# Kernel tuning notes

Measured on AMD Instinct MI355X. Metric: run time of the kernel, lower is better.

Reference implementation:

```python
import jax, jax.numpy as jnp
import numpy as np

EPS = 1e-5
NEG_SLOPE = 0.2

def _conv1x1(x, w):
    # x: (B,C,N,K), w: (O,C) -> (B,O,N,K)
    return jnp.einsum('oc,bcnk->bonk', w, x)

def _bn(x, g, b, m, v):
    scale = g / jnp.sqrt(v + EPS)
    return x * scale[None, :, None, None] + (b - m * scale)[None, :, None, None]

def _lrelu(x):
    return jnp.where(x > 0, x, NEG_SLOPE * x)

def setup_inputs() -> dict:
    key = jax.random.key(0)
    specs = {
        'x': ((8, 6, 8192, 20), 'randn'),
        'trans_w': ((64, 6), 'randn'), 'trans_g': ((64,), 'rand'), 'trans_b': ((64,), 'randn'),
        'trans_m': ((64,), 'randn'), 'trans_v': ((64,), 'rand'),
        'pos_w1': ((64, 3), 'randn'), 'pos_g': ((64,), 'rand'), 'pos_b': ((64,), 'randn'),
        'pos_m': ((64,), 'randn'), 'pos_v': ((64,), 'rand'),
        'pos_w2': ((64, 64), 'randn'), 'pos_b2': ((64,), 'randn'),
        'gate_w1': ((16, 6), 'randn'), 'gate_g': ((16,), 'rand'), 'gate_b': ((16,), 'randn'),
        'gate_m': ((16,), 'randn'), 'gate_v': ((16,), 'rand'),
        'gate_w2': ((1, 16), 'randn'), 'gate_b2': ((1,), 'ones'),
        'attn_w1': ((16, 6), 'randn'), 'attn_g': ((16,), 'rand'), 'attn_b': ((16,), 'randn'),
        'attn_m': ((16,), 'randn'), 'attn_v': ((16,), 'rand'),
        'attn_w2': ((64, 16), 'randn'), 'attn_b2': ((64,), 'randn'),
    }
    out = {}
    for i, (name, (shape, fill)) in enumerate(specs.items()):
        k = jax.random.fold_in(key, i)
        if fill == 'randn':
            out[name] = jax.random.normal(k, shape, dtype=jnp.float32) * 0.1
        elif fill == 'rand':
            out[name] = jax.random.uniform(k, shape, dtype=jnp.float32)
        else:  # ones (gate bias init to 2.0 in original; scale ones)
            out[name] = jnp.ones(shape, dtype=jnp.float32) * 2.0
    return out

def reference(x, trans_w, trans_g, trans_b, trans_m, trans_v,
              pos_w1, pos_g, pos_b, pos_m, pos_v, pos_w2, pos_b2,
              gate_w1, gate_g, gate_b, gate_m, gate_v, gate_w2, gate_b2,
              attn_w1, attn_g, attn_b, attn_m, attn_v, attn_w2, attn_b2):
    in_channels = 3
    rel_pos = x[:, in_channels:in_channels + 3, :, :]  # (B,3,N,K)
    # pos_net: conv(3->C) + BN + LReLU + conv(C->C, bias)
    pos_h = _lrelu(_bn(_conv1x1(rel_pos, pos_w1), pos_g, pos_b, pos_m, pos_v))
    pos_enc = _conv1x1(pos_h, pos_w2) + pos_b2[None, :, None, None]
    # trans: conv(2*Cin->C) + BN + LReLU
    trans_feat = _lrelu(_bn(_conv1x1(x, trans_w), trans_g, trans_b, trans_m, trans_v)) + pos_enc
    # gate_net: conv(6->16)+BN+LReLU+conv(16->1,bias)+sigmoid (dropout=0 in eval)
    gate_h = _lrelu(_bn(_conv1x1(x, gate_w1), gate_g, gate_b, gate_m, gate_v))
    gate_map = jax.nn.sigmoid(_conv1x1(gate_h, gate_w2) + gate_b2[None, :, None, None])  # (B,1,N,K)
    clean_feat = trans_feat * gate_map
    # attn_net: conv(6->16)+BN+LReLU+conv(16->C,bias), then + pos_enc, softmax over K
    attn_h = _lrelu(_bn(_conv1x1(x, attn_w1), attn_g, attn_b, attn_m, attn_v))
    attn_logits = _conv1x1(attn_h, attn_w2) + attn_b2[None, :, None, None] + pos_enc
    attn_weights = jax.nn.softmax(attn_logits, axis=-1)
    out_attn = (trans_feat * attn_weights).sum(axis=-1)  # (B,C,N)
    out_max = clean_feat.max(axis=-1)                    # (B,C,N)
    return out_attn + out_max
```

## Files before the change

kernel.cpp:

```cpp
#include <hip/hip_runtime.h>
#include <math.h>

#define NEG 0.2f
#define EPSV 1e-5f

typedef _Float16 v8h __attribute__((ext_vector_type(8)));
typedef _Float16 v4h __attribute__((ext_vector_type(4)));
typedef float    v4f __attribute__((ext_vector_type(4)));

__device__ __forceinline__ float lrelu(float v) { return fmaxf(v, NEG * v); }

#define MFMA(a, b, c) __builtin_amdgcn_mfma_f32_16x16x32_f16((a), (b), (c), 0, 0, 0)

__global__ __launch_bounds__(256, 1)
void gsl_mfma(const float* __restrict__ x,
              const float* __restrict__ trans_w, const float* __restrict__ trans_g,
              const float* __restrict__ trans_b, const float* __restrict__ trans_m,
              const float* __restrict__ trans_v,
              const float* __restrict__ pos_w1, const float* __restrict__ pos_g,
              const float* __restrict__ pos_b, const float* __restrict__ pos_m,
              const float* __restrict__ pos_v, const float* __restrict__ pos_w2,
              const float* __restrict__ pos_b2,
              const float* __restrict__ gate_w1, const float* __restrict__ gate_g,
              const float* __restrict__ gate_b, const float* __restrict__ gate_m,
              const float* __restrict__ gate_v, const float* __restrict__ gate_w2,
              const float* __restrict__ gate_b2,
              const float* __restrict__ attn_w1, const float* __restrict__ attn_g,
              const float* __restrict__ attn_b, const float* __restrict__ attn_m,
              const float* __restrict__ attn_v, const float* __restrict__ attn_w2,
              const float* __restrict__ attn_b2,
              float* __restrict__ out)
{
    __shared__ _Float16 PHB[4][1280];
    __shared__ _Float16 AHB[4][448];

    const int tid  = threadIdx.x;
    const int wv   = tid >> 6;
    const int lane = tid & 63;
    const int p    = lane & 15;
    const int q    = lane >> 4;

    const int b = blockIdx.x >> 7;
    const int n = ((blockIdx.x & 127) << 6) | (wv << 4) | p;

    v8h W2f[4][2], WTf[4], WP1f[4], WA2f[4], WA1f, WG1f;
    v4f pb2v[4];
    #pragma unroll
    for (int mt = 0; mt < 4; ++mt) {
        const int ch = mt * 16 + p;
        #pragma unroll
        for (int h = 0; h < 2; ++h)
            #pragma unroll
            for (int i = 0; i < 8; ++i)
                W2f[mt][h][i] = (_Float16)pos_w2[ch * 64 + h * 32 + q * 8 + i];
        #pragma unroll
        for (int i = 0; i < 8; ++i) {
            int k = q * 8 + i;
            WA2f[mt][i] = (k < 16) ? (_Float16)attn_w2[ch * 16 + k] : (_Float16)0.f;
        }
        {
            float st = trans_g[ch] * rsqrtf(trans_v[ch] + EPSV);
            float bt = trans_b[ch] - trans_m[ch] * st;
            #pragma unroll
            for (int i = 0; i < 8; ++i) {
                int k = q * 8 + i;
                float v = (k < 6) ? trans_w[ch * 6 + k] * st : ((k == 6) ? bt : 0.f);
                WTf[mt][i] = (_Float16)v;
            }
        }
        {
            float sp = pos_g[ch] * rsqrtf(pos_v[ch] + EPSV);
            float bp = pos_b[ch] - pos_m[ch] * sp;
            #pragma unroll
            for (int i = 0; i < 8; ++i) {
                int k = q * 8 + i;
                float v = (k >= 3 && k < 6) ? pos_w1[ch * 3 + (k - 3)] * sp
                                            : ((k == 6) ? bp : 0.f);
                WP1f[mt][i] = (_Float16)v;
            }
        }
        #pragma unroll
        for (int r = 0; r < 4; ++r)
            pb2v[mt][r] = pos_b2[mt * 16 + 4 * q + r];
    }
    {
        float sa = attn_g[p] * rsqrtf(attn_v[p] + EPSV);
        float ba = attn_b[p] - attn_m[p] * sa;
        #pragma unroll
        for (int i = 0; i < 8; ++i) {
            int k = q * 8 + i;
            float v = (k < 6) ? attn_w1[p * 6 + k] * sa : ((k == 6) ? ba : 0.f);
            WA1f[i] = (_Float16)v;
        }
    }
    {
        float sg = gate_g[p] * rsqrtf(gate_v[p] + EPSV);
        float bg = gate_b[p] - gate_m[p] * sg;
        #pragma unroll
        for (int i = 0; i < 8; ++i) {
            int k = q * 8 + i;
            float v = (k < 6) ? gate_w1[p * 6 + k] * sg : ((k == 6) ? bg : 0.f);
            WG1f[i] = (_Float16)v;
        }
    }
    float g2w[4];
    #pragma unroll
    for (int r = 0; r < 4; ++r) g2w[r] = gate_w2[4 * q + r];
    const float gb2v = gate_b2[0];

    _Float16* PH = PHB[wv];
    _Float16* AH = AHB[wv];

    const v4f zero = {0.f, 0.f, 0.f, 0.f};
    v4f den[4], num[4], cmx[4];
    #pragma unroll
    for (int mt = 0; mt < 4; ++mt) {
        den[mt] = zero; num[mt] = zero;
        cmx[mt] = (v4f){-3.4e38f, -3.4e38f, -3.4e38f, -3.4e38f};
    }

    const float* xb = x + ((size_t)(b * 6) * 8192 + n) * 20;
    float nx[6];
    #pragma unroll
    for (int c = 0; c < 6; ++c) nx[c] = xb[(size_t)c * 163840];

    #pragma unroll 1
    for (int k = 0; k < 20; ++k) {
        v8h xvf;
        #pragma unroll
        for (int c = 0; c < 6; ++c) xvf[c] = (_Float16)nx[c];
        xvf[6] = (_Float16)1.f;
        xvf[7] = (_Float16)0.f;
        const int kn = (k < 19) ? k + 1 : 19;
        #pragma unroll
        for (int c = 0; c < 6; ++c) nx[c] = xb[(size_t)c * 163840 + kn];

        v4f tfa[4], php[4];
        #pragma unroll
        for (int mt = 0; mt < 4; ++mt) tfa[mt] = MFMA(WTf[mt], xvf, zero);
        #pragma unroll
        for (int mt = 0; mt < 4; ++mt) php[mt] = MFMA(WP1f[mt], xvf, zero);
        v4f ahp = MFMA(WA1f, xvf, zero);
        v4f ghp = MFMA(WG1f, xvf, zero);

        #pragma unroll
        for (int mt = 0; mt < 4; ++mt) {
            v4h v;
            #pragma unroll
            for (int r = 0; r < 4; ++r) v[r] = (_Float16)lrelu(php[mt][r]);
            *(v4h*)(PH + p * 80 + mt * 16 + 4 * q) = v;
        }
        {
            v4h v;
            #pragma unroll
            for (int r = 0; r < 4; ++r) v[r] = (_Float16)lrelu(ahp[r]);
            *(v4h*)(AH + p * 24 + 4 * q) = v;
        }

        float ga = 0.f;
        #pragma unroll
        for (int r = 0; r < 4; ++r) ga += g2w[r] * lrelu(ghp[r]);
        ga += __shfl_xor(ga, 16);
        ga += __shfl_xor(ga, 32);
        const float gate = 1.f / (1.f + __expf(-(ga + gb2v)));

        v8h phf0 = *(const v8h*)(PH + p * 80 + 8 * q);
        v8h phf1 = *(const v8h*)(PH + p * 80 + 32 + 8 * q);
        v8h ahf  = *(const v8h*)(AH + p * 24 + 8 * q);

        v4f pe[4];
        #pragma unroll
        for (int mt = 0; mt < 4; ++mt) {
            pe[mt] = MFMA(W2f[mt][0], phf0, pb2v[mt]);
            pe[mt] = MFMA(W2f[mt][1], phf1, pe[mt]);
        }

        #pragma unroll
        for (int mt = 0; mt < 4; ++mt) {
            v4f tfv;
            #pragma unroll
            for (int r = 0; r < 4; ++r) tfv[r] = lrelu(tfa[mt][r]) + pe[mt][r];
            pe[mt] = MFMA(WA2f[mt], ahf, pe[mt]);
            #pragma unroll
            for (int r = 0; r < 4; ++r) {
                float e = __expf(pe[mt][r]);
                den[mt][r] += e;
                num[mt][r] += tfv[r] * e;
                cmx[mt][r] = fmaxf(cmx[mt][r], tfv[r] * gate);
            }
        }
    }

    #pragma unroll
    for (int mt = 0; mt < 4; ++mt) {
        #pragma unroll
        for (int r = 0; r < 4; ++r) {
            const int ch = mt * 16 + 4 * q + r;
            out[((size_t)(b * 64 + ch)) * 8192 + n] =
                num[mt][r] / den[mt][r] + cmx[mt][r];
        }
    }
}

extern "C" void kernel_launch(void* const* d_in, const int* in_sizes, int n_in,
                              void* d_out, int out_size, void* d_ws, size_t ws_size,
                              hipStream_t stream) {
    const float* x       = (const float*)d_in[0];
    const float* trans_w = (const float*)d_in[1];
    const float* trans_g = (const float*)d_in[2];
    const float* trans_b = (const float*)d_in[3];
    const float* trans_m = (const float*)d_in[4];
    const float* trans_v = (const float*)d_in[5];
    const float* pos_w1  = (const float*)d_in[6];
    const float* pos_g   = (const float*)d_in[7];
    const float* pos_b   = (const float*)d_in[8];
    const float* pos_m   = (const float*)d_in[9];
    const float* pos_v   = (const float*)d_in[10];
    const float* pos_w2  = (const float*)d_in[11];
    const float* pos_b2  = (const float*)d_in[12];
    const float* gate_w1 = (const float*)d_in[13];
    const float* gate_g  = (const float*)d_in[14];
    const float* gate_b  = (const float*)d_in[15];
    const float* gate_m  = (const float*)d_in[16];
    const float* gate_v  = (const float*)d_in[17];
    const float* gate_w2 = (const float*)d_in[18];
    const float* gate_b2 = (const float*)d_in[19];
    const float* attn_w1 = (const float*)d_in[20];
    const float* attn_g  = (const float*)d_in[21];
    const float* attn_b  = (const float*)d_in[22];
    const float* attn_m  = (const float*)d_in[23];
    const float* attn_v  = (const float*)d_in[24];
    const float* attn_w2 = (const float*)d_in[25];
    const float* attn_b2 = (const float*)d_in[26];
    float* out = (float*)d_out;

    gsl_mfma<<<1024, 256, 0, stream>>>(
        x, trans_w, trans_g, trans_b, trans_m, trans_v,
        pos_w1, pos_g, pos_b, pos_m, pos_v, pos_w2, pos_b2,
        gate_w1, gate_g, gate_b, gate_m, gate_v, gate_w2, gate_b2,
        attn_w1, attn_g, attn_b, attn_m, attn_v, attn_w2, attn_b2,
        out);
}
```

Measured before the change: 209.9 us.

## Double-buffer hidden-activation LDS tiles to software-pipeline the K loop

Splits the per-wave LDS scratch for the pos and attn hidden activations into two buffers. The first-layer MFMAs and LDS writes for step k+1 are issued while step k reads its already-written buffer, so the LDS write-to-read dependency leaves the critical path of each iteration. It also uses packed cvt_pkrtz conversions to fp16, which round toward zero instead of to nearest, and shrinks the PH row stride from 80 to 72 halves. The costs are more LDS and registers, plus a one-time zeroing of the AH buffers.

After: 206.6 us. No clear change (-1.6%).

```diff
diff --git a/kernel.cpp b/kernel.cpp
--- a/kernel.cpp
+++ b/kernel.cpp
@@ -6,9 +6,17 @@
 
 typedef _Float16 v8h __attribute__((ext_vector_type(8)));
 typedef _Float16 v4h __attribute__((ext_vector_type(4)));
+typedef _Float16 v2h __attribute__((ext_vector_type(2)));
+typedef __fp16   f16x2 __attribute__((ext_vector_type(2)));
 typedef float    v4f __attribute__((ext_vector_type(4)));
 
 __device__ __forceinline__ float lrelu(float v) { return fmaxf(v, NEG * v); }
+
+__device__ __forceinline__ v2h pk(float a, float b) {
+    union { f16x2 i; v2h o; } u;
+    u.i = __builtin_amdgcn_cvt_pkrtz(a, b);
+    return u.o;
+}
 
 #define MFMA(a, b, c) __builtin_amdgcn_mfma_f32_16x16x32_f16((a), (b), (c), 0, 0, 0)
 
@@ -31,8 +39,8 @@
               const float* __restrict__ attn_b2,
               float* __restrict__ out)
 {
-    __shared__ _Float16 PHB[4][1280];
-    __shared__ _Float16 AHB[4][448];
+    __shared__ _Float16 PHB[4][2][1152];
+    __shared__ _Float16 AHB[4][2][448];
 
     const int tid  = threadIdx.x;
     const int wv   = tid >> 6;
@@ -43,6 +51,12 @@
     const int b = blockIdx.x >> 7;
     const int n = ((blockIdx.x & 127) << 6) | (wv << 4) | p;
 
+    {
+        _Float16* AH0 = &AHB[wv][0][0];
+        const v4h zh = {(_Float16)0.f, (_Float16)0.f, (_Float16)0.f, (_Float16)0.f};
+        for (int i = lane; i < 224; i += 64) *(v4h*)(AH0 + 4 * i) = zh;
+    }
+
     v8h W2f[4][2], WTf[4], WP1f[4], WA2f[4], WA1f, WG1f;
     v4f pb2v[4];
     #pragma unroll
@@ -108,8 +122,8 @@
     for (int r = 0; r < 4; ++r) g2w[r] = gate_w2[4 * q + r];
     const float gb2v = gate_b2[0];
 
-    _Float16* PH = PHB[wv];
-    _Float16* AH = AHB[wv];
+    _Float16* const PHbase = &PHB[wv][0][0];
+    _Float16* const AHbase = &AHB[wv][0][0];
 
     const v4f zero = {0.f, 0.f, 0.f, 0.f};
     v4f den[4], num[4], cmx[4];
@@ -120,53 +134,91 @@
     }
 
     const float* xb = x + ((size_t)(b * 6) * 8192 + n) * 20;
+
     float nx[6];
     #pragma unroll
     for (int c = 0; c < 6; ++c) nx[c] = xb[(size_t)c * 163840];
+
+    v8h xv_cur;
+    {
+        union { v8h v; v2h h[4]; } u;
+        u.h[0] = pk(nx[0], nx[1]);
+        u.h[1] = pk(nx[2], nx[3]);
+        u.h[2] = pk(nx[4], nx[5]);
+        u.h[3] = (v2h){(_Float16)1.f, (_Float16)0.f};
+        xv_cur = u.v;
+    }
+    #pragma unroll
+    for (int c = 0; c < 6; ++c) nx[c] = xb[(size_t)c * 163840 + 1];
+
+    {
+        v4f php[4];
+        #pragma unroll
+        for (int mt = 0; mt < 4; ++mt) php[mt] = MFMA(WP1f[mt], xv_cur, zero);
+        v4f ahp = MFMA(WA1f, xv_cur, zero);
+        _Float16* PHW = PHbase + p * 72 + 4 * q;
+        #pragma unroll
+        for (int mt = 0; mt < 4; ++mt) {
+            union { v4h v; v2h h[2]; } u;
+            u.h[0] = pk(lrelu(php[mt][0]), lrelu(php[mt][1]));
+            u.h[1] = pk(lrelu(php[mt][2]), lrelu(php[mt][3]));
+            *(v4h*)(PHW + mt * 16) = u.v;
+        }
+        union { v4h v; v2h h[2]; } ua;
+        ua.h[0] = pk(lrelu(ahp[0]), lrelu(ahp[1]));
+        ua.h[1] = pk(lrelu(ahp[2]), lrelu(ahp[3]));
+        *(v4h*)(AHbase + p * 24 + 4 * q) = ua.v;
+    }
 
     #pragma unroll 1
     for (int k = 0; k < 20; ++k) {
-        v8h xvf;
-        #pragma unroll
-        for (int c = 0; c < 6; ++c) xvf[c] = (_Float16)nx[c];
-        xvf[6] = (_Float16)1.f;
-        xvf[7] = (_Float16)0.f;
-        const int kn = (k < 19) ? k + 1 : 19;
-        #pragma unroll
-        for (int c = 0; c < 6; ++c) nx[c] = xb[(size_t)c * 163840 + kn];
-
-        v4f tfa[4], php[4];
-        #pragma unroll
-        for (int mt = 0; mt < 4; ++mt) tfa[mt] = MFMA(WTf[mt], xvf, zero);
-        #pragma unroll
-        for (int mt = 0; mt < 4; ++mt) php[mt] = MFMA(WP1f[mt], xvf, zero);
-        v4f ahp = MFMA(WA1f, xvf, zero);
-        v4f ghp = MFMA(WG1f, xvf, zero);
-
-        #pragma unroll
-        for (int mt = 0; mt < 4; ++mt) {
-            v4h v;
-            #pragma unroll
-            for (int r = 0; r < 4; ++r) v[r] = (_Float16)lrelu(php[mt][r]);
-            *(v4h*)(PH + p * 80 + mt * 16 + 4 * q) = v;
-        }
-        {
-            v4h v;
-            #pragma unroll
-            for (int r = 0; r < 4; ++r) v[r] = (_Float16)lrelu(ahp[r]);
-            *(v4h*)(AH + p * 24 + 4 * q) = v;
-        }
-
+        const int sel = k & 1;
+        _Float16* PH = PHbase + sel * 1152;
+        _Float16* AH = AHbase + sel * 448;
+        v8h phf0 = *(const v8h*)(PH + p * 72 + 8 * q);
+        v8h phf1 = *(const v8h*)(PH + p * 72 + 32 + 8 * q);
+        v8h ahf  = *(const v8h*)(AH + p * 24 + 8 * q);
+
+        v8h xv_nxt = xv_cur;
+        if (k < 19) {
+            union { v8h v; v2h h[4]; } u;
+            u.h[0] = pk(nx[0], nx[1]);
+            u.h[1] = pk(nx[2], nx[3]);
+            u.h[2] = pk(nx[4], nx[5]);
+            u.h[3] = (v2h){(_Float16)1.f, (_Float16)0.f};
+            xv_nxt = u.v;
+            const int kn = (k < 18) ? k + 2 : 19;
+            #pragma unroll
+            for (int c = 0; c < 6; ++c) nx[c] = xb[(size_t)c * 163840 + kn];
+
+            v4f php[4];
+            #pragma unroll
+            for (int mt = 0; mt < 4; ++mt) php[mt] = MFMA(WP1f[mt], xv_nxt, zero);
+            v4f ahp = MFMA(WA1f, xv_nxt, zero);
+            _Float16* PHW = PHbase + (sel ^ 1) * 1152 + p * 72 + 4 * q;
+            #pragma unroll
+            for (int mt = 0; mt < 4; ++mt) {
+                union { v4h v; v2h h[2]; } uu;
+                uu.h[0] = pk(lrelu(php[mt][0]), lrelu(php[mt][1]));
+                uu.h[1] = pk(lrelu(php[mt][2]), lrelu(php[mt][3]));
+                *(v4h*)(PHW + mt * 16) = uu.v;
+            }
+            union { v4h v; v2h h[2]; } ua;
+            ua.h[0] = pk(lrelu(ahp[0]), lrelu(ahp[1]));
+            ua.h[1] = pk(lrelu(ahp[2]), lrelu(ahp[3]));
+            *(v4h*)(AHbase + (sel ^ 1) * 448 + p * 24 + 4 * q) = ua.v;
+        }
+
+        v4f tfa[4];
+        #pragma unroll
+        for (int mt = 0; mt < 4; ++mt) tfa[mt] = MFMA(WTf[mt], xv_cur, zero);
+        v4f ghp = MFMA(WG1f, xv_cur, zero);
         float ga = 0.f;
         #pragma unroll
         for (int r = 0; r < 4; ++r) ga += g2w[r] * lrelu(ghp[r]);
         ga += __shfl_xor(ga, 16);
         ga += __shfl_xor(ga, 32);
         const float gate = 1.f / (1.f + __expf(-(ga + gb2v)));
-
-        v8h phf0 = *(const v8h*)(PH + p * 80 + 8 * q);
-        v8h phf1 = *(const v8h*)(PH + p * 80 + 32 + 8 * q);
-        v8h ahf  = *(const v8h*)(AH + p * 24 + 8 * q);
 
         v4f pe[4];
         #pragma unroll
@@ -189,6 +241,7 @@
                 cmx[mt][r] = fmaxf(cmx[mt][r], tfv[r] * gate);
             }
         }
+        xv_cur = xv_nxt;
     }
 
     #pragma unroll
```
